# Kernel optimization log

Hardware: AMD Instinct MI355X
Metric: run time of the kernel (lower is better)

The kernel has to match this reference:

```python
import jax, jax.numpy as jnp
import numpy as np

B, S, D = 4, 2048, 256
H = 8
HD = D // H
DFF = 512
EPS_CUTOFF = 1e-15
LN_EPS = 1e-5


def _layer_norm(x, gamma, beta):
    mu = jnp.mean(x, axis=-1, keepdims=True)
    var = jnp.mean(jnp.square(x - mu), axis=-1, keepdims=True)
    return (x - mu) * jax.lax.rsqrt(var + LN_EPS) * gamma + beta


def setup_inputs() -> dict:
    key = jax.random.key(0)
    ks = jax.random.split(key, 12)
    s = 1.0 / np.sqrt(D)
    inp = {
        "tokens": jax.random.normal(ks[0], (B, S, D), dtype=jnp.float32),
        "cutoff_factors": jax.random.uniform(ks[1], (B, S, S), dtype=jnp.float32),
        "Wqkv": jax.random.uniform(ks[2], (3 * D, D), jnp.float32, -s, s),
        "bqkv": jnp.zeros((3 * D,), jnp.float32),
        "Wo": jax.random.uniform(ks[3], (D, D), jnp.float32, -s, s),
        "bo": jnp.zeros((D,), jnp.float32),
        "ln1_g": jnp.ones((D,), jnp.float32),
        "ln1_b": jnp.zeros((D,), jnp.float32),
        "ln2_g": jnp.ones((D,), jnp.float32),
        "ln2_b": jnp.zeros((D,), jnp.float32),
        "W1": jax.random.uniform(ks[4], (DFF, D), jnp.float32, -s, s),
        "b1": jax.random.uniform(ks[5], (DFF,), jnp.float32, -s, s),
        "W2": jax.random.uniform(ks[6], (D, DFF), jnp.float32, -1.0 / np.sqrt(DFF), 1.0 / np.sqrt(DFF)),
        "b2": jax.random.uniform(ks[7], (D,), jnp.float32, -1.0 / np.sqrt(DFF), 1.0 / np.sqrt(DFF)),
        "use_manual_attention": 1,
    }
    return inp


def reference(tokens, cutoff_factors, Wqkv, bqkv, Wo, bo, ln1_g, ln1_b, ln2_g, ln2_b, W1, b1, W2, b2, use_manual_attention):
    # --- attention block ---
    qkv = tokens @ Wqkv.T + bqkv                      # [B,S,3D]
    qkv = qkv.reshape(B, S, 3, H, HD).transpose(2, 0, 3, 1, 4)  # [3,B,H,S,HD]
    q, k, v = qkv[0], qkv[1], qkv[2]
    attn_mask = jnp.log(jnp.clip(cutoff_factors, EPS_CUTOFF))[:, None, :, :]  # [B,1,S,S]
    scores = jnp.einsum("bhqd,bhkd->bhqk", q, k) / np.sqrt(HD) + attn_mask
    probs = jax.nn.softmax(scores, axis=-1)
    attn = jnp.einsum("bhqk,bhkd->bhqd", probs, v)    # [B,H,S,HD]
    attn = attn.transpose(0, 2, 1, 3).reshape(B, S, D)
    attn = attn @ Wo.T + bo
    # --- PostLN residual + norm ---
    x = _layer_norm(tokens + attn, ln1_g, ln1_b)
    # --- MLP (SiLU) ---
    h = jax.nn.silu(x @ W1.T + b1)
    mlp_out = h @ W2.T + b2
    return _layer_norm(x + mlp_out, ln2_g, ln2_b)
```

## Files before the change

kernel.cpp:

```cpp
#include <hip/hip_runtime.h>
#include <hip/hip_bf16.h>
#include <math.h>

#define B_ 4
#define S_ 2048
#define D_ 256
#define H_ 8
#define HD_ 32
#define DFF_ 512

typedef __attribute__((ext_vector_type(8))) short bf16x8;
typedef __attribute__((ext_vector_type(4))) float f32x4;

__device__ inline short f2bf(float f) {
  union { float f; unsigned u; } x; x.f = f;
  unsigned r = (x.u + 0x7FFFu + ((x.u >> 16) & 1u)) >> 16;
  return (short)r;
}
__device__ inline float bf2f(short s) {
  union { unsigned u; float f; } x; x.u = ((unsigned)(unsigned short)s) << 16;
  return x.f;
}
__device__ inline unsigned cvt_pk_bf16(float a, float b) {
  unsigned r;
  asm("v_cvt_pk_bf16_f32 %0, %1, %2" : "=v"(r) : "v"(a), "v"(b));
  return r;
}
__device__ inline float exp2v(float x) {
  float r;
  asm("v_exp_f32 %0, %1" : "=v"(r) : "v"(x));
  return r;
}

__global__ __launch_bounds__(256) void cvt_all(const float* __restrict__ tok, const float* __restrict__ wq,
                                               const float* __restrict__ wo, const float* __restrict__ w1,
                                               const float* __restrict__ w2,
                                               short* __restrict__ dtok, short* __restrict__ dwq,
                                               short* __restrict__ dwo, short* __restrict__ dw1,
                                               short* __restrict__ dw2) {
  int blk = blockIdx.x;
  const float* src; short* dst; int base;
  if (blk < 2048)      { src = tok; dst = dtok; base = blk; }
  else if (blk < 2240) { src = wq;  dst = dwq;  base = blk - 2048; }
  else if (blk < 2304) { src = wo;  dst = dwo;  base = blk - 2240; }
  else if (blk < 2432) { src = w1;  dst = dw1;  base = blk - 2304; }
  else                 { src = w2;  dst = dw2;  base = blk - 2432; }
  int i = (base * 256 + threadIdx.x) * 4;
  float4 v = *(const float4*)(src + i);
  short4 s; s.x = f2bf(v.x); s.y = f2bf(v.y); s.z = f2bf(v.z); s.w = f2bf(v.w);
  *(short4*)(dst + i) = s;
}

template<int MODE>
__global__ __launch_bounds__(256) void gemm_bf(const short* __restrict__ A,
                                               const short* __restrict__ W,
                                               const float* __restrict__ bias,
                                               float* __restrict__ Cf,
                                               short* __restrict__ Cb,
                                               unsigned* __restrict__ kmaxp,
                                               int M, int N, int K) {
  constexpr int BM = 128, BN = 64;
  __shared__ short As[BM][72];
  __shared__ short Bs[BN][72];
  const int tid = threadIdx.x;
  const int wid = tid >> 6, lane = tid & 63;
  const int g = lane >> 4, lc = lane & 15;
  const int wr = wid >> 1, wc = wid & 1;
  const int rowBase = blockIdx.y * BM;
  const int colBase = blockIdx.x * BN;

  f32x4 acc[4][2];
#pragma unroll
  for (int m = 0; m < 4; ++m)
#pragma unroll
    for (int n = 0; n < 2; ++n) { acc[m][n][0]=0.f; acc[m][n][1]=0.f; acc[m][n][2]=0.f; acc[m][n][3]=0.f; }

  for (int k0 = 0; k0 < K; k0 += 64) {
    __syncthreads();
#pragma unroll
    for (int i = 0; i < 4; ++i) {
      int task = tid + 256 * i;
      int r = task >> 3, c = (task & 7) * 8;
      *(bf16x8*)&As[r][c] = *(const bf16x8*)(A + (size_t)(rowBase + r) * K + k0 + c);
    }
#pragma unroll
    for (int i = 0; i < 2; ++i) {
      int task = tid + 256 * i;
      int r = task >> 3, c = (task & 7) * 8;
      *(bf16x8*)&Bs[r][c] = *(const bf16x8*)(W + (size_t)(colBase + r) * K + k0 + c);
    }
    __syncthreads();
#pragma unroll
    for (int ks = 0; ks < 2; ++ks) {
      bf16x8 af[4], bfr[2];
#pragma unroll
      for (int m = 0; m < 4; ++m) af[m] = *(const bf16x8*)&As[wr*64 + m*16 + lc][ks*32 + g*8];
#pragma unroll
      for (int n = 0; n < 2; ++n) bfr[n] = *(const bf16x8*)&Bs[wc*32 + n*16 + lc][ks*32 + g*8];
#pragma unroll
      for (int m = 0; m < 4; ++m)
#pragma unroll
        for (int n = 0; n < 2; ++n)
          acc[m][n] = __builtin_amdgcn_mfma_f32_16x16x32_bf16(af[m], bfr[n], acc[m][n], 0, 0, 0);
    }
  }

  const int part = (colBase + wc * 32) >> 8;
  float rmax = 0.f;
#pragma unroll
  for (int m = 0; m < 4; ++m) {
    float nsum[4] = {0.f, 0.f, 0.f, 0.f};
#pragma unroll
    for (int n = 0; n < 2; ++n) {
      int col = colBase + wc*32 + n*16 + lc;
      float bv = bias[col];
      int row0 = rowBase + wr*64 + m*16 + g*4;
      float vj[4];
#pragma unroll
      for (int j = 0; j < 4; ++j) vj[j] = acc[m][n][j] + bv;
      if (MODE == 1) {
#pragma unroll
        for (int j = 0; j < 4; ++j) {
          float v = vj[j];
          v = v / (1.f + __expf(-v));
          Cb[(size_t)(row0 + j) * N + col] = f2bf(v);
        }
      } else {
        int h = (col >> 5) & 7;
        int hd = col & 31;
        int b = row0 >> 11, s0 = row0 & 2047;
        if (part == 2) {
          short4 s4;
          s4.x = f2bf(vj[0]); s4.y = f2bf(vj[1]); s4.z = f2bf(vj[2]); s4.w = f2bf(vj[3]);
          *(short4*)(Cb + 2 * 2097152 + (((size_t)b * 8 + h) * 32 + hd) * 2048 + s0) = s4;
        } else {
          float sc = (part == 0) ? 0.25506807f : 1.f;
#pragma unroll
          for (int j = 0; j < 4; ++j)
            Cb[(size_t)part * 2097152 + (((size_t)b * 8 + h) * 2048 + s0 + j) * 32 + hd] = f2bf(vj[j] * sc);
          if (part == 1) {
#pragma unroll
            for (int j = 0; j < 4; ++j) nsum[j] = fmaf(vj[j], vj[j], nsum[j]);
          }
        }
      }
    }
    if (MODE == 2 && part == 1) {
#pragma unroll
      for (int j = 0; j < 4; ++j) {
        float t = nsum[j];
        t += __shfl_xor(t, 1, 64); t += __shfl_xor(t, 2, 64);
        t += __shfl_xor(t, 4, 64); t += __shfl_xor(t, 8, 64);
        rmax = fmaxf(rmax, t);
      }
    }
  }
  if (MODE == 2 && part == 1) {
    rmax = fmaxf(rmax, __shfl_xor(rmax, 16, 64));
    rmax = fmaxf(rmax, __shfl_xor(rmax, 32, 64));
    if (lane == 0) {
      int h = ((colBase + wc * 32) >> 5) & 7;
      int b = rowBase >> 11;
      atomicMax(kmaxp + b * 8 + h, __float_as_uint(rmax));
    }
  }
}

__global__ __launch_bounds__(256) void gemm_bf64(const short* __restrict__ A,
                                                 const short* __restrict__ W,
                                                 const float* __restrict__ bias,
                                                 float* __restrict__ Cf,
                                                 int M, int N, int K) {
  __shared__ short As[64][72];
  __shared__ short Bs[64][72];
  const int tid = threadIdx.x;
  const int wid = tid >> 6, lane = tid & 63;
  const int g = lane >> 4, lc = lane & 15;
  const int wr = wid >> 1, wc = wid & 1;
  const int rowBase = blockIdx.y * 64;
  const int colBase = blockIdx.x * 64;

  f32x4 acc[2][2];
#pragma unroll
  for (int m = 0; m < 2; ++m)
#pragma unroll
    for (int n = 0; n < 2; ++n) { acc[m][n][0]=0.f; acc[m][n][1]=0.f; acc[m][n][2]=0.f; acc[m][n][3]=0.f; }

  for (int k0 = 0; k0 < K; k0 += 64) {
    __syncthreads();
#pragma unroll
    for (int i = 0; i < 2; ++i) {
      int task = tid + 256 * i;
      int r = task >> 3, c = (task & 7) * 8;
      *(bf16x8*)&As[r][c] = *(const bf16x8*)(A + (size_t)(rowBase + r) * K + k0 + c);
      *(bf16x8*)&Bs[r][c] = *(const bf16x8*)(W + (size_t)(colBase + r) * K + k0 + c);
    }
    __syncthreads();
#pragma unroll
    for (int ks = 0; ks < 2; ++ks) {
      bf16x8 af[2], bfr[2];
#pragma unroll
      for (int m = 0; m < 2; ++m) af[m] = *(const bf16x8*)&As[wr*32 + m*16 + lc][ks*32 + g*8];
#pragma unroll
      for (int n = 0; n < 2; ++n) bfr[n] = *(const bf16x8*)&Bs[wc*32 + n*16 + lc][ks*32 + g*8];
#pragma unroll
      for (int m = 0; m < 2; ++m)
#pragma unroll
        for (int n = 0; n < 2; ++n)
          acc[m][n] = __builtin_amdgcn_mfma_f32_16x16x32_bf16(af[m], bfr[n], acc[m][n], 0, 0, 0);
    }
  }

#pragma unroll
  for (int m = 0; m < 2; ++m)
#pragma unroll
    for (int n = 0; n < 2; ++n) {
      int col = colBase + wc*32 + n*16 + lc;
      float bv = bias[col];
      int row0 = rowBase + wr*32 + m*16 + g*4;
#pragma unroll
      for (int j = 0; j < 4; ++j)
        Cf[(size_t)(row0 + j) * N + col] = acc[m][n][j] + bv;
    }
}

__global__ __launch_bounds__(256, 4) void attn_mfma(const short* __restrict__ qbf,
                                                    const short* __restrict__ kbf,
                                                    const short* __restrict__ vtbf,
                                                    const float* __restrict__ cutoff,
                                                    const unsigned* __restrict__ kmaxp,
                                                    short* __restrict__ outbf) {
  constexpr int KB = 64;
  const int qt = blockIdx.x & 31;
  const int h  = (blockIdx.x >> 5) & 7;
  const int b  = blockIdx.x >> 8;
  const int tid = threadIdx.x;
  const int wid = tid >> 6, lane = tid & 63;
  const int g = lane >> 4, lc = lane & 15;

  __shared__ __align__(16) short Ks[2][KB][32];
  __shared__ __align__(16) short Vt[2][HD_][72];
  __shared__ __align__(16) short Pq[4][16][72];

  const int bh = b * H_ + h;
  const int qrow = qt * 64 + wid * 16 + lc;
  const short* qg = qbf + (size_t)bh * S_ * HD_;
  const short* kg = kbf + (size_t)bh * S_ * HD_;
  const short* vg = vtbf + (size_t)bh * HD_ * S_;

  bf16x8 qf = *(const bf16x8*)(qg + (size_t)qrow * HD_ + g * 8);

  float ssq = 0.f;
#pragma unroll
  for (int i = 0; i < 8; ++i) { float f = bf2f(qf[i]); ssq = fmaf(f, f, ssq); }
  ssq += __shfl_xor(ssq, 16, 64);
  ssq += __shfl_xor(ssq, 32, 64);
  const float m = sqrtf(ssq * __uint_as_float(kmaxp[bh]));

  f32x4 oacc[2];
#pragma unroll
  for (int d = 0; d < 2; ++d) { oacc[d][0]=0.f; oacc[d][1]=0.f; oacc[d][2]=0.f; oacc[d][3]=0.f; }
  float sml = 0.f;

  const float* cb = cutoff + ((size_t)(b * S_) + qrow) * (size_t)S_;

  const int kr = tid >> 2;
  const int kslot = ((tid & 3) ^ ((kr >> 1) & 3)) * 8;
  const short* kptr = kg + (size_t)kr * HD_ + (tid & 3) * 8;
  const int vr = tid >> 3;
  const int vc = (tid & 7) * 8;
  const short* vptr = vg + (size_t)vr * S_ + vc;

  bf16x8 kreg = *(const bf16x8*)kptr;
  bf16x8 vreg = *(const bf16x8*)vptr;
  *(bf16x8*)&Ks[0][kr][kslot] = kreg;
  *(bf16x8*)&Vt[0][vr][vc] = vreg;
  float4 cv[4];
#pragma unroll
  for (int t = 0; t < 4; ++t) cv[t] = *(const float4*)(cb + t * 16 + g * 4);
  __syncthreads();

  int cur = 0;
#pragma unroll 2
  for (int kt = 0; kt < S_; kt += KB) {
    const bool notlast = (kt + KB < S_);
    if (notlast) {
      kreg = *(const bf16x8*)(kptr + (size_t)(kt + KB) * HD_);
      vreg = *(const bf16x8*)(vptr + (kt + KB));
    }

    bf16x8 kf[4];
#pragma unroll
    for (int t = 0; t < 4; ++t)
      kf[t] = *(const bf16x8*)&Ks[cur][t*16 + lc][(g ^ ((lc >> 1) & 3)) * 8];
    f32x4 st[4];
#pragma unroll
    for (int t = 0; t < 4; ++t) {
      f32x4 z = {0.f, 0.f, 0.f, 0.f};
      st[t] = __builtin_amdgcn_mfma_f32_16x16x32_bf16(kf[t], qf, z, 0, 0, 0);
    }

    float4 cvn[4];
    if (notlast) {
#pragma unroll
      for (int t = 0; t < 4; ++t) cvn[t] = *(const float4*)(cb + kt + KB + t * 16 + g * 4);
    }

#pragma unroll
    for (int t = 0; t < 4; ++t) {
      float p0 = cv[t].x * exp2v(fminf(st[t][0] - m, 8.f));
      float p1 = cv[t].y * exp2v(fminf(st[t][1] - m, 8.f));
      float p2 = cv[t].z * exp2v(fminf(st[t][2] - m, 8.f));
      float p3 = cv[t].w * exp2v(fminf(st[t][3] - m, 8.f));
      sml += (p0 + p1) + (p2 + p3);
      uint2 pk;
      pk.x = cvt_pk_bf16(p0, p1);
      pk.y = cvt_pk_bf16(p2, p3);
      *(uint2*)&Pq[wid][lc][t*16 + g*4] = pk;
    }

    asm volatile("s_waitcnt lgkmcnt(0)" ::: "memory");
    __builtin_amdgcn_sched_barrier(0);

#pragma unroll
    for (int kh = 0; kh < 2; ++kh) {
      bf16x8 pb = *(const bf16x8*)&Pq[wid][lc][kh*32 + g*8];
#pragma unroll
      for (int dh = 0; dh < 2; ++dh) {
        bf16x8 va = *(const bf16x8*)&Vt[cur][dh*16 + lc][kh*32 + g*8];
        oacc[dh] = __builtin_amdgcn_mfma_f32_16x16x32_bf16(va, pb, oacc[dh], 0, 0, 0);
      }
    }

    if (notlast) {
      __syncthreads();
      *(bf16x8*)&Ks[cur ^ 1][kr][kslot] = kreg;
      *(bf16x8*)&Vt[cur ^ 1][vr][vc] = vreg;
      __syncthreads();
      cur ^= 1;
#pragma unroll
      for (int t = 0; t < 4; ++t) cv[t] = cvn[t];
    }
  }

  float s = sml;
  s += __shfl_xor(s, 16, 64);
  s += __shfl_xor(s, 32, 64);
  float inv = 1.f / s;
#pragma unroll
  for (int dh = 0; dh < 2; ++dh) {
    uint2 pk;
    pk.x = cvt_pk_bf16(oacc[dh][0] * inv, oacc[dh][1] * inv);
    pk.y = cvt_pk_bf16(oacc[dh][2] * inv, oacc[dh][3] * inv);
    *(uint2*)(outbf + ((size_t)(b * S_) + qrow) * D_ + h * HD_ + dh * 16 + g * 4) = pk;
  }
}

template<int WBF>
__global__ __launch_bounds__(256) void residual_ln(const float* __restrict__ xa,
                                                   const float* __restrict__ xb,
                                                   const float* __restrict__ g,
                                                   const float* __restrict__ bt,
                                                   float* __restrict__ out,
                                                   short* __restrict__ outbf) {
  const int row  = blockIdx.x * 4 + (threadIdx.x >> 6);
  const int lane = threadIdx.x & 63;
  float4 va = *(const float4*)(xa + (size_t)row * D_ + lane * 4);
  float4 vb = *(const float4*)(xb + (size_t)row * D_ + lane * 4);
  float v[4] = {va.x + vb.x, va.y + vb.y, va.z + vb.z, va.w + vb.w};
  float s = v[0] + v[1] + v[2] + v[3];
#pragma unroll
  for (int o = 32; o > 0; o >>= 1) s += __shfl_xor(s, o, 64);
  float mu = s * (1.f / D_);
  float var = 0.f;
#pragma unroll
  for (int i = 0; i < 4; ++i) { v[i] -= mu; var += v[i] * v[i]; }
#pragma unroll
  for (int o = 32; o > 0; o >>= 1) var += __shfl_xor(var, o, 64);
  float rs = rsqrtf(var * (1.f / D_) + 1e-5f);
  float4 g4 = *(const float4*)(g + lane * 4);
  float4 b4 = *(const float4*)(bt + lane * 4);
  float4 o4 = {v[0] * rs * g4.x + b4.x, v[1] * rs * g4.y + b4.y,
               v[2] * rs * g4.z + b4.z, v[3] * rs * g4.w + b4.w};
  *(float4*)(out + (size_t)row * D_ + lane * 4) = o4;
  if (WBF) {
    short4 s4; s4.x = f2bf(o4.x); s4.y = f2bf(o4.y); s4.z = f2bf(o4.z); s4.w = f2bf(o4.w);
    *(short4*)(outbf + (size_t)row * D_ + lane * 4) = s4;
  }
}

extern "C" void kernel_launch(void* const* d_in, const int* in_sizes, int n_in,
                              void* d_out, int out_size, void* d_ws, size_t ws_size,
                              hipStream_t stream) {
  const float* tokens = (const float*)d_in[0];
  const float* cutoff = (const float*)d_in[1];
  const float* Wqkv   = (const float*)d_in[2];
  const float* bqkv   = (const float*)d_in[3];
  const float* Wo     = (const float*)d_in[4];
  const float* bo     = (const float*)d_in[5];
  const float* ln1g   = (const float*)d_in[6];
  const float* ln1b   = (const float*)d_in[7];
  const float* ln2g   = (const float*)d_in[8];
  const float* ln2b   = (const float*)d_in[9];
  const float* W1     = (const float*)d_in[10];
  const float* b1     = (const float*)d_in[11];
  const float* W2     = (const float*)d_in[12];
  const float* b2     = (const float*)d_in[13];
  float* out = (float*)d_out;

  char* w = (char*)d_ws;
  const size_t MB = 1 << 20;
  short* qbf    = (short*)w;
  short* kbf    = qbf + 2097152;
  short* vtbf   = qbf + 2 * 2097152;
  short* tokbf  = (short*)(w + 12 * MB);
  short* wq_bf  = (short*)(w + 16 * MB);
  short* wo_bf  = wq_bf + 196608;
  short* w1_bf  = wo_bf + 65536;
  short* w2_bf  = w1_bf + 131072;
  short* attnbf = tokbf;
  float* projOut = (float*)(w + 18 * MB);
  float* xbuf    = (float*)(w + 26 * MB);
  unsigned* kmax = (unsigned*)(w + 34 * MB);
  short* xbbf    = qbf;
  short* hbbf    = kbf;
  float* mlpOut  = projOut;

  const int M = B_ * S_;

  hipMemsetAsync(kmax, 0, 128, stream);
  cvt_all<<<dim3(2560), 256, 0, stream>>>(tokens, Wqkv, Wo, W1, W2, tokbf, wq_bf, wo_bf, w1_bf, w2_bf);

  gemm_bf<2><<<dim3(12, 64), 256, 0, stream>>>(tokbf, wq_bf, bqkv, nullptr, qbf, kmax, M, 3 * D_, D_);
  attn_mfma<<<dim3(1024), 256, 0, stream>>>(qbf, kbf, vtbf, cutoff, kmax, attnbf);
  gemm_bf64<<<dim3(4, 128), 256, 0, stream>>>(attnbf, wo_bf, bo, projOut, M, D_, D_);
  residual_ln<1><<<dim3(M / 4), 256, 0, stream>>>(tokens, projOut, ln1g, ln1b, xbuf, xbbf);
  gemm_bf<1><<<dim3(8, 64), 256, 0, stream>>>(xbbf, w1_bf, b1, nullptr, hbbf, nullptr, M, DFF_, D_);
  gemm_bf64<<<dim3(4, 128), 256, 0, stream>>>(hbbf, w2_bf, b2, mlpOut, M, D_, DFF_);
  residual_ln<0><<<dim3(M / 4), 256, 0, stream>>>(xbuf, mlpOut, ln2g, ln2b, out, nullptr);
}
```

Measured before the change: 145.2 us.

## Split attention over key halves with combine kernel; fuse token conversion into QKV GEMM

Attention blocks now each process half of the key sequence, writing unnormalized fp32 partial outputs and row sums, and a new combine kernel adds the halves and normalizes to bf16. This doubles the block count to improve occupancy and latency hiding, with launch bounds raised to 6 blocks per CU. The token fp32-to-bf16 conversion is folded into the QKV GEMM's A-tile load, removing a separate pass. The trade-off is extra global traffic for fp32 partials and an added kernel launch.

```diff
diff --git a/kernel.cpp b/kernel.cpp
--- a/kernel.cpp
+++ b/kernel.cpp
@@ -32,19 +32,18 @@
   return r;
 }
 
-__global__ __launch_bounds__(256) void cvt_all(const float* __restrict__ tok, const float* __restrict__ wq,
-                                               const float* __restrict__ wo, const float* __restrict__ w1,
-                                               const float* __restrict__ w2,
-                                               short* __restrict__ dtok, short* __restrict__ dwq,
-                                               short* __restrict__ dwo, short* __restrict__ dw1,
-                                               short* __restrict__ dw2) {
+__global__ __launch_bounds__(256) void cvt_w(const float* __restrict__ wq,
+                                             const float* __restrict__ wo, const float* __restrict__ w1,
+                                             const float* __restrict__ w2,
+                                             short* __restrict__ dwq,
+                                             short* __restrict__ dwo, short* __restrict__ dw1,
+                                             short* __restrict__ dw2) {
   int blk = blockIdx.x;
   const float* src; short* dst; int base;
-  if (blk < 2048)      { src = tok; dst = dtok; base = blk; }
-  else if (blk < 2240) { src = wq;  dst = dwq;  base = blk - 2048; }
-  else if (blk < 2304) { src = wo;  dst = dwo;  base = blk - 2240; }
-  else if (blk < 2432) { src = w1;  dst = dw1;  base = blk - 2304; }
-  else                 { src = w2;  dst = dw2;  base = blk - 2432; }
+  if (blk < 192)      { src = wq; dst = dwq; base = blk; }
+  else if (blk < 256) { src = wo; dst = dwo; base = blk - 192; }
+  else if (blk < 384) { src = w1; dst = dw1; base = blk - 256; }
+  else                { src = w2; dst = dw2; base = blk - 384; }
   int i = (base * 256 + threadIdx.x) * 4;
   float4 v = *(const float4*)(src + i);
   short4 s; s.x = f2bf(v.x); s.y = f2bf(v.y); s.z = f2bf(v.z); s.w = f2bf(v.w);
@@ -53,9 +52,9 @@
 
 template<int MODE>
 __global__ __launch_bounds__(256) void gemm_bf(const short* __restrict__ A,
+                                               const float* __restrict__ Af,
                                                const short* __restrict__ W,
                                                const float* __restrict__ bias,
-                                               float* __restrict__ Cf,
                                                short* __restrict__ Cb,
                                                unsigned* __restrict__ kmaxp,
                                                int M, int N, int K) {
@@ -81,7 +80,19 @@
     for (int i = 0; i < 4; ++i) {
       int task = tid + 256 * i;
       int r = task >> 3, c = (task & 7) * 8;
-      *(bf16x8*)&As[r][c] = *(const bf16x8*)(A + (size_t)(rowBase + r) * K + k0 + c);
+      if (MODE == 2) {
+        const float* ap = Af + (size_t)(rowBase + r) * K + k0 + c;
+        float4 v0 = *(const float4*)ap;
+        float4 v1 = *(const float4*)(ap + 4);
+        union { unsigned u[4]; bf16x8 v; } t;
+        t.u[0] = cvt_pk_bf16(v0.x, v0.y);
+        t.u[1] = cvt_pk_bf16(v0.z, v0.w);
+        t.u[2] = cvt_pk_bf16(v1.x, v1.y);
+        t.u[3] = cvt_pk_bf16(v1.z, v1.w);
+        *(bf16x8*)&As[r][c] = t.v;
+      } else {
+        *(bf16x8*)&As[r][c] = *(const bf16x8*)(A + (size_t)(rowBase + r) * K + k0 + c);
+      }
     }
 #pragma unroll
     for (int i = 0; i < 2; ++i) {
@@ -224,16 +235,20 @@
     }
 }
 
-__global__ __launch_bounds__(256, 4) void attn_mfma(const short* __restrict__ qbf,
+__global__ __launch_bounds__(256, 6) void attn_mfma(const short* __restrict__ qbf,
                                                     const short* __restrict__ kbf,
                                                     const short* __restrict__ vtbf,
                                                     const float* __restrict__ cutoff,
                                                     const unsigned* __restrict__ kmaxp,
-                                                    short* __restrict__ outbf) {
+                                                    float* __restrict__ po,
+                                                    float* __restrict__ ps) {
   constexpr int KB = 64;
-  const int qt = blockIdx.x & 31;
-  const int h  = (blockIdx.x >> 5) & 7;
-  const int b  = blockIdx.x >> 8;
+  constexpr int KSP = S_ / 2;
+  const int half = blockIdx.x & 1;
+  const int rest = blockIdx.x >> 1;
+  const int qt = rest & 31;
+  const int h  = (rest >> 5) & 7;
+  const int b  = rest >> 8;
   const int tid = threadIdx.x;
   const int wid = tid >> 6, lane = tid & 63;
   const int g = lane >> 4, lc = lane & 15;
@@ -245,8 +260,8 @@
   const int bh = b * H_ + h;
   const int qrow = qt * 64 + wid * 16 + lc;
   const short* qg = qbf + (size_t)bh * S_ * HD_;
-  const short* kg = kbf + (size_t)bh * S_ * HD_;
-  const short* vg = vtbf + (size_t)bh * HD_ * S_;
+  const short* kg = kbf + (size_t)bh * S_ * HD_ + (size_t)half * KSP * HD_;
+  const short* vg = vtbf + (size_t)bh * HD_ * S_ + half * KSP;
 
   bf16x8 qf = *(const bf16x8*)(qg + (size_t)qrow * HD_ + g * 8);
 
@@ -262,7 +277,7 @@
   for (int d = 0; d < 2; ++d) { oacc[d][0]=0.f; oacc[d][1]=0.f; oacc[d][2]=0.f; oacc[d][3]=0.f; }
   float sml = 0.f;
 
-  const float* cb = cutoff + ((size_t)(b * S_) + qrow) * (size_t)S_;
+  const float* cb = cutoff + ((size_t)(b * S_) + qrow) * (size_t)S_ + half * KSP;
 
   const int kr = tid >> 2;
   const int kslot = ((tid & 3) ^ ((kr >> 1) & 3)) * 8;
@@ -282,8 +297,8 @@
 
   int cur = 0;
 #pragma unroll 2
-  for (int kt = 0; kt < S_; kt += KB) {
-    const bool notlast = (kt + KB < S_);
+  for (int kt = 0; kt < KSP; kt += KB) {
+    const bool notlast = (kt + KB < KSP);
     if (notlast) {
       kreg = *(const bf16x8*)(kptr + (size_t)(kt + KB) * HD_);
       vreg = *(const bf16x8*)(vptr + (kt + KB));
@@ -346,14 +361,27 @@
   float s = sml;
   s += __shfl_xor(s, 16, 64);
   s += __shfl_xor(s, 32, 64);
-  float inv = 1.f / s;
-#pragma unroll
-  for (int dh = 0; dh < 2; ++dh) {
-    uint2 pk;
-    pk.x = cvt_pk_bf16(oacc[dh][0] * inv, oacc[dh][1] * inv);
-    pk.y = cvt_pk_bf16(oacc[dh][2] * inv, oacc[dh][3] * inv);
-    *(uint2*)(outbf + ((size_t)(b * S_) + qrow) * D_ + h * HD_ + dh * 16 + g * 4) = pk;
-  }
+  if (g == 0) ps[half * 65536 + bh * S_ + qrow] = s;
+  float* pop = po + (size_t)half * 2097152 + ((size_t)(b * S_) + qrow) * D_ + h * HD_;
+#pragma unroll
+  for (int dh = 0; dh < 2; ++dh)
+    *(f32x4*)(pop + dh * 16 + g * 4) = oacc[dh];
+}
+
+__global__ __launch_bounds__(256) void attn_combine(const float* __restrict__ po,
+                                                    const float* __restrict__ ps,
+                                                    short* __restrict__ outbf) {
+  int i = (blockIdx.x * 256 + threadIdx.x) * 4;
+  int row = i >> 8;
+  int col = i & 255;
+  int bhq = ((row >> 11) * 8 + (col >> 5)) * 2048 + (row & 2047);
+  float inv = 1.f / (ps[bhq] + ps[65536 + bhq]);
+  float4 a = *(const float4*)(po + i);
+  float4 c = *(const float4*)(po + 2097152 + i);
+  uint2 pk;
+  pk.x = cvt_pk_bf16((a.x + c.x) * inv, (a.y + c.y) * inv);
+  pk.y = cvt_pk_bf16((a.z + c.z) * inv, (a.w + c.w) * inv);
+  *(uint2*)(outbf + i) = pk;
 }
 
 template<int WBF>
@@ -413,15 +441,16 @@
   short* qbf    = (short*)w;
   short* kbf    = qbf + 2097152;
   short* vtbf   = qbf + 2 * 2097152;
-  short* tokbf  = (short*)(w + 12 * MB);
+  short* attnbf = (short*)(w + 12 * MB);
   short* wq_bf  = (short*)(w + 16 * MB);
   short* wo_bf  = wq_bf + 196608;
   short* w1_bf  = wo_bf + 65536;
   short* w2_bf  = w1_bf + 131072;
-  short* attnbf = tokbf;
+  float* po     = (float*)(w + 18 * MB);
   float* projOut = (float*)(w + 18 * MB);
   float* xbuf    = (float*)(w + 26 * MB);
-  unsigned* kmax = (unsigned*)(w + 34 * MB);
+  float* ps      = (float*)(w + 34 * MB);
+  unsigned* kmax = (unsigned*)(w + 34 * MB + 524288);
   short* xbbf    = qbf;
   short* hbbf    = kbf;
   float* mlpOut  = projOut;
@@ -429,13 +458,14 @@
   const int M = B_ * S_;
 
   hipMemsetAsync(kmax, 0, 128, stream);
-  cvt_all<<<dim3(2560), 256, 0, stream>>>(tokens, Wqkv, Wo, W1, W2, tokbf, wq_bf, wo_bf, w1_bf, w2_bf);
-
-  gemm_bf<2><<<dim3(12, 64), 256, 0, stream>>>(tokbf, wq_bf, bqkv, nullptr, qbf, kmax, M, 3 * D_, D_);
-  attn_mfma<<<dim3(1024), 256, 0, stream>>>(qbf, kbf, vtbf, cutoff, kmax, attnbf);
+  cvt_w<<<dim3(512), 256, 0, stream>>>(Wqkv, Wo, W1, W2, wq_bf, wo_bf, w1_bf, w2_bf);
+
+  gemm_bf<2><<<dim3(12, 64), 256, 0, stream>>>(nullptr, tokens, wq_bf, bqkv, qbf, kmax, M, 3 * D_, D_);
+  attn_mfma<<<dim3(2048), 256, 0, stream>>>(qbf, kbf, vtbf, cutoff, kmax, po, ps);
+  attn_combine<<<dim3(2048), 256, 0, stream>>>(po, ps, attnbf);
   gemm_bf64<<<dim3(4, 128), 256, 0, stream>>>(attnbf, wo_bf, bo, projOut, M, D_, D_);
   residual_ln<1><<<dim3(M / 4), 256, 0, stream>>>(tokens, projOut, ln1g, ln1b, xbuf, xbbf);
-  gemm_bf<1><<<dim3(8, 64), 256, 0, stream>>>(xbbf, w1_bf, b1, nullptr, hbbf, nullptr, M, DFF_, D_);
+  gemm_bf<1><<<dim3(8, 64), 256, 0, stream>>>(xbbf, nullptr, w1_bf, b1, hbbf, nullptr, M, DFF_, D_);
   gemm_bf64<<<dim3(4, 128), 256, 0, stream>>>(hbbf, w2_bf, b2, mlpOut, M, D_, DFF_);
   residual_ln<0><<<dim3(M / 4), 256, 0, stream>>>(xbuf, mlpOut, ln2g, ln2b, out, nullptr);
 }
```

New measurement: 273.3 us. +88.2%, slower.

## Fuse token bf16 conversion into QKV GEMM and deepen cutoff prefetch

Applied to the files above, without the earlier changes.

The QKV GEMM now reads fp32 tokens directly and converts them to bf16 while staging into shared memory, so the separate token conversion pass and its bf16 intermediate buffer are gone. The weight conversion kernel shrinks to cover only the weights. The attention kernel also prefetches the cutoff-factor tiles two iterations ahead using a double-buffered register array, to hide global load latency on the large S×S mask stream. In exchange, the GEMM's A loads move twice the bytes and there is extra register pressure in attention.

```diff
diff --git a/kernel.cpp b/kernel.cpp
--- a/kernel.cpp
+++ b/kernel.cpp
@@ -32,19 +32,18 @@
   return r;
 }
 
-__global__ __launch_bounds__(256) void cvt_all(const float* __restrict__ tok, const float* __restrict__ wq,
-                                               const float* __restrict__ wo, const float* __restrict__ w1,
-                                               const float* __restrict__ w2,
-                                               short* __restrict__ dtok, short* __restrict__ dwq,
-                                               short* __restrict__ dwo, short* __restrict__ dw1,
-                                               short* __restrict__ dw2) {
+__global__ __launch_bounds__(256) void cvt_w(const float* __restrict__ wq,
+                                             const float* __restrict__ wo, const float* __restrict__ w1,
+                                             const float* __restrict__ w2,
+                                             short* __restrict__ dwq,
+                                             short* __restrict__ dwo, short* __restrict__ dw1,
+                                             short* __restrict__ dw2) {
   int blk = blockIdx.x;
   const float* src; short* dst; int base;
-  if (blk < 2048)      { src = tok; dst = dtok; base = blk; }
-  else if (blk < 2240) { src = wq;  dst = dwq;  base = blk - 2048; }
-  else if (blk < 2304) { src = wo;  dst = dwo;  base = blk - 2240; }
-  else if (blk < 2432) { src = w1;  dst = dw1;  base = blk - 2304; }
-  else                 { src = w2;  dst = dw2;  base = blk - 2432; }
+  if (blk < 192)      { src = wq; dst = dwq; base = blk; }
+  else if (blk < 256) { src = wo; dst = dwo; base = blk - 192; }
+  else if (blk < 384) { src = w1; dst = dw1; base = blk - 256; }
+  else                { src = w2; dst = dw2; base = blk - 384; }
   int i = (base * 256 + threadIdx.x) * 4;
   float4 v = *(const float4*)(src + i);
   short4 s; s.x = f2bf(v.x); s.y = f2bf(v.y); s.z = f2bf(v.z); s.w = f2bf(v.w);
@@ -53,9 +52,9 @@
 
 template<int MODE>
 __global__ __launch_bounds__(256) void gemm_bf(const short* __restrict__ A,
+                                               const float* __restrict__ Af,
                                                const short* __restrict__ W,
                                                const float* __restrict__ bias,
-                                               float* __restrict__ Cf,
                                                short* __restrict__ Cb,
                                                unsigned* __restrict__ kmaxp,
                                                int M, int N, int K) {
@@ -81,7 +80,19 @@
     for (int i = 0; i < 4; ++i) {
       int task = tid + 256 * i;
       int r = task >> 3, c = (task & 7) * 8;
-      *(bf16x8*)&As[r][c] = *(const bf16x8*)(A + (size_t)(rowBase + r) * K + k0 + c);
+      if (MODE == 2) {
+        const float* ap = Af + (size_t)(rowBase + r) * K + k0 + c;
+        float4 v0 = *(const float4*)ap;
+        float4 v1 = *(const float4*)(ap + 4);
+        union { unsigned u[4]; bf16x8 v; } t;
+        t.u[0] = cvt_pk_bf16(v0.x, v0.y);
+        t.u[1] = cvt_pk_bf16(v0.z, v0.w);
+        t.u[2] = cvt_pk_bf16(v1.x, v1.y);
+        t.u[3] = cvt_pk_bf16(v1.z, v1.w);
+        *(bf16x8*)&As[r][c] = t.v;
+      } else {
+        *(bf16x8*)&As[r][c] = *(const bf16x8*)(A + (size_t)(rowBase + r) * K + k0 + c);
+      }
     }
 #pragma unroll
     for (int i = 0; i < 2; ++i) {
@@ -275,15 +286,28 @@
   bf16x8 vreg = *(const bf16x8*)vptr;
   *(bf16x8*)&Ks[0][kr][kslot] = kreg;
   *(bf16x8*)&Vt[0][vr][vc] = vreg;
-  float4 cv[4];
-#pragma unroll
-  for (int t = 0; t < 4; ++t) cv[t] = *(const float4*)(cb + t * 16 + g * 4);
+  float4 cvbuf[2][4];
+#pragma unroll
+  for (int t = 0; t < 4; ++t) cvbuf[0][t] = *(const float4*)(cb + t * 16 + g * 4);
+#pragma unroll
+  for (int t = 0; t < 4; ++t) cvbuf[1][t] = *(const float4*)(cb + KB + t * 16 + g * 4);
   __syncthreads();
 
   int cur = 0;
 #pragma unroll 2
   for (int kt = 0; kt < S_; kt += KB) {
     const bool notlast = (kt + KB < S_);
+    const int par = (kt >> 6) & 1;
+
+    float4 cv[4];
+#pragma unroll
+    for (int t = 0; t < 4; ++t) cv[t] = cvbuf[par][t];
+    if (kt + 2 * KB < S_) {
+#pragma unroll
+      for (int t = 0; t < 4; ++t)
+        cvbuf[par][t] = *(const float4*)(cb + kt + 2 * KB + t * 16 + g * 4);
+    }
+
     if (notlast) {
       kreg = *(const bf16x8*)(kptr + (size_t)(kt + KB) * HD_);
       vreg = *(const bf16x8*)(vptr + (kt + KB));
@@ -298,12 +322,6 @@
     for (int t = 0; t < 4; ++t) {
       f32x4 z = {0.f, 0.f, 0.f, 0.f};
       st[t] = __builtin_amdgcn_mfma_f32_16x16x32_bf16(kf[t], qf, z, 0, 0, 0);
-    }
-
-    float4 cvn[4];
-    if (notlast) {
-#pragma unroll
-      for (int t = 0; t < 4; ++t) cvn[t] = *(const float4*)(cb + kt + KB + t * 16 + g * 4);
     }
 
 #pragma unroll
@@ -338,8 +356,6 @@
       *(bf16x8*)&Vt[cur ^ 1][vr][vc] = vreg;
       __syncthreads();
       cur ^= 1;
-#pragma unroll
-      for (int t = 0; t < 4; ++t) cv[t] = cvn[t];
     }
   }
 
@@ -413,12 +429,11 @@
   short* qbf    = (short*)w;
   short* kbf    = qbf + 2097152;
   short* vtbf   = qbf + 2 * 2097152;
-  short* tokbf  = (short*)(w + 12 * MB);
+  short* attnbf = (short*)(w + 12 * MB);
   short* wq_bf  = (short*)(w + 16 * MB);
   short* wo_bf  = wq_bf + 196608;
   short* w1_bf  = wo_bf + 65536;
   short* w2_bf  = w1_bf + 131072;
-  short* attnbf = tokbf;
   float* projOut = (float*)(w + 18 * MB);
   float* xbuf    = (float*)(w + 26 * MB);
   unsigned* kmax = (unsigned*)(w + 34 * MB);
@@ -429,13 +444,13 @@
   const int M = B_ * S_;
 
   hipMemsetAsync(kmax, 0, 128, stream);
-  cvt_all<<<dim3(2560), 256, 0, stream>>>(tokens, Wqkv, Wo, W1, W2, tokbf, wq_bf, wo_bf, w1_bf, w2_bf);
-
-  gemm_bf<2><<<dim3(12, 64), 256, 0, stream>>>(tokbf, wq_bf, bqkv, nullptr, qbf, kmax, M, 3 * D_, D_);
+  cvt_w<<<dim3(512), 256, 0, stream>>>(Wqkv, Wo, W1, W2, wq_bf, wo_bf, w1_bf, w2_bf);
+
+  gemm_bf<2><<<dim3(12, 64), 256, 0, stream>>>(nullptr, tokens, wq_bf, bqkv, qbf, kmax, M, 3 * D_, D_);
   attn_mfma<<<dim3(1024), 256, 0, stream>>>(qbf, kbf, vtbf, cutoff, kmax, attnbf);
   gemm_bf64<<<dim3(4, 128), 256, 0, stream>>>(attnbf, wo_bf, bo, projOut, M, D_, D_);
   residual_ln<1><<<dim3(M / 4), 256, 0, stream>>>(tokens, projOut, ln1g, ln1b, xbuf, xbbf);
-  gemm_bf<1><<<dim3(8, 64), 256, 0, stream>>>(xbbf, w1_bf, b1, nullptr, hbbf, nullptr, M, DFF_, D_);
+  gemm_bf<1><<<dim3(8, 64), 256, 0, stream>>>(xbbf, nullptr, w1_bf, b1, hbbf, nullptr, M, DFF_, D_);
   gemm_bf64<<<dim3(4, 128), 256, 0, stream>>>(hbbf, w2_bf, b2, mlpOut, M, D_, DFF_);
   residual_ln<0><<<dim3(M / 4), 256, 0, stream>>>(xbuf, mlpOut, ln2g, ln2b, out, nullptr);
 }
```

Measured after the change: 151.8 us. +4.5%, slower.
